# Kernel tuning notes

Hardware: AMD Instinct MI355X
Metric: run time of the kernel (lower is better)

## Reference

```python
import jax, jax.numpy as jnp
import numpy as np

ALPHA = 0.1
DEPTH = 10

N_NODES = 100000
N_EDGES = 3200000
FEATS = 512
HIDDEN = 64
CLASSES = 32


def setup_inputs() -> dict:
    key = jax.random.key(0)
    k1, k2, k3, k4 = jax.random.split(key, 4)
    x = jax.random.normal(k1, (N_NODES, FEATS), dtype=jnp.float32)
    edges = jax.random.randint(k2, (2, N_EDGES), 0, N_NODES, dtype=jnp.int64)
    # Linear weights (stored as [in, out] so forward is x @ W + b)
    W1 = jax.random.normal(k3, (FEATS, HIDDEN), dtype=jnp.float32) * (1.0 / np.sqrt(FEATS))
    b1 = jnp.zeros((HIDDEN,), dtype=jnp.float32)
    W2 = jax.random.normal(k4, (HIDDEN, CLASSES), dtype=jnp.float32) * (1.0 / np.sqrt(HIDDEN))
    b2 = jnp.zeros((CLASSES,), dtype=jnp.float32)
    return {"x": x, "edges": edges, "W1": W1, "b1": b1, "W2": W2, "b2": b2}


def reference(x, edges, W1, b1, W2, b2):
    # Eval mode: all dropouts (feature + edge) are identity.
    n = x.shape[0]
    src, dst = edges[0], edges[1]

    # Symmetric normalization 1/sqrt(deg_src * deg_dst), degrees from in-edges.
    deg = jax.ops.segment_sum(jnp.ones_like(dst, dtype=x.dtype), dst, num_segments=n)
    deg = jnp.maximum(deg, 1.0)
    norm = jax.lax.rsqrt(deg[src] * deg[dst])  # [E]

    # MLP: feats -> hidden -> classes
    h = jax.nn.relu(x @ W1 + b1) @ W2 + b2  # [N, classes]
    h0 = h

    # APPNP propagation: x <- (1-alpha) * A_hat x + alpha * h0
    for _ in range(DEPTH):
        msg = h[src] * norm[:, None]                          # gather  [E, classes]
        agg = jax.ops.segment_sum(msg, dst, num_segments=n)   # scatter [N, classes]
        h = agg * (1.0 - ALPHA) + ALPHA * h0
    return h
```

## Files before the change

kernel.cpp:

```cpp
#include <hip/hip_runtime.h>

#define ALPHA_F 0.1f
#define DEPTH 10
#define FEATS 512
#define CLS 32

__device__ __forceinline__ unsigned bf16rne(float f) {
  unsigned u = __float_as_uint(f);
  return (u + 0x7fffu + ((u >> 16) & 1u)) >> 16;
}
__device__ __forceinline__ float blo(unsigned q) { return __uint_as_float(q << 16); }
__device__ __forceinline__ float bhi(unsigned q) { return __uint_as_float(q & 0xffff0000u); }

__global__ __launch_bounds__(256) void k_deg(const int* __restrict__ dst, int E, int N,
                                             unsigned* __restrict__ deg,
                                             unsigned* __restrict__ rank) {
  int i = blockIdx.x * 256 + threadIdx.x;
  if (i >= E) return;
  int d = dst[i];
  unsigned r = 0;
  if ((unsigned)d < (unsigned)N) r = atomicAdd(&deg[d], 1u);
  rank[i] = r;
}

__global__ __launch_bounds__(1024) void k_scanp(const unsigned* __restrict__ deg, int N,
                                                unsigned* __restrict__ rowst2) {
  __shared__ unsigned sums[1024];
  int t = threadIdx.x;
  int chunk = (N + 1023) >> 10;
  int beg = t * chunk;
  int end = min(beg + chunk, N);
  unsigned s = 0;
  for (int i = beg; i < end; ++i) s += (deg[i] + 15u) & ~15u;
  sums[t] = s;
  __syncthreads();
  for (int off = 1; off < 1024; off <<= 1) {
    unsigned v = (t >= off) ? sums[t - off] : 0u;
    __syncthreads();
    sums[t] += v;
    __syncthreads();
  }
  unsigned pre = (t == 0) ? 0u : sums[t - 1];
  for (int i = beg; i < end; ++i) { rowst2[i] = pre; pre += (deg[i] + 15u) & ~15u; }
  if (t == 1023) rowst2[N] = pre;
}

__global__ __launch_bounds__(256) void k_colinit(unsigned* __restrict__ col2, int cap, int N) {
  int i = blockIdx.x * 256 + threadIdx.x;
  if (i < cap) col2[i] = (unsigned)N;
}

__global__ __launch_bounds__(256) void k_fill(const int* __restrict__ src,
                                              const int* __restrict__ dst,
                                              const unsigned* __restrict__ rank,
                                              const unsigned* __restrict__ rowst2,
                                              int E, int N,
                                              unsigned* __restrict__ col2) {
  int e = blockIdx.x * 256 + threadIdx.x;
  if (e >= E) return;
  int s = src[e];
  int d = dst[e];
  if ((unsigned)s >= (unsigned)N || (unsigned)d >= (unsigned)N) return;
  col2[rowst2[d] + rank[e]] = (unsigned)s;
}

__global__ __launch_bounds__(256) void k_mlp(const float* __restrict__ x,
                                             const float* __restrict__ W1,
                                             const float* __restrict__ b1,
                                             const float* __restrict__ W2,
                                             const float* __restrict__ b2,
                                             const unsigned* __restrict__ deg,
                                             unsigned short* __restrict__ h0b,
                                             unsigned short* __restrict__ u0,
                                             float* __restrict__ rs, int N) {
  __shared__ float XHs[64 * 65];
  __shared__ float W2s[64 * 32];
  __shared__ float b1s[64];
  __shared__ float b2s[32];
  int t = threadIdx.x;
  int m0 = blockIdx.x * 64;

  for (int i = t; i < 64 * 32; i += 256) W2s[i] = W2[i];
  if (t < 64) b1s[t] = b1[t];
  if (t < 32) b2s[t] = b2[t];

  int c = t & 31;
  int h = t >> 5;
  float acc[8][2];
#pragma unroll
  for (int i = 0; i < 8; ++i) { acc[i][0] = 0.f; acc[i][1] = 0.f; }

  for (int k0 = 0; k0 < FEATS; k0 += 64) {
    __syncthreads();
#pragma unroll
    for (int j = 0; j < 2; ++j) {
      int F = j * 256 + t;
      int r = F >> 3, q = F & 7;
      int row = m0 + r;
      float4 v = make_float4(0.f, 0.f, 0.f, 0.f);
      if (row < N) v = *(const float4*)(x + (size_t)row * FEATS + k0 + q * 8);
      *(float4*)(XHs + r * 64 + q * 8) = v;
      float4 v2 = make_float4(0.f, 0.f, 0.f, 0.f);
      if (row < N) v2 = *(const float4*)(x + (size_t)row * FEATS + k0 + q * 8 + 4);
      *(float4*)(XHs + r * 64 + q * 8 + 4) = v2;
    }
    __syncthreads();
    const float* W1p = W1 + (size_t)k0 * 64;
#pragma unroll
    for (int k4 = 0; k4 < 16; ++k4) {
      int k = k4 * 4;
      float4 xv[8];
#pragma unroll
      for (int i = 0; i < 8; ++i) xv[i] = *(const float4*)(XHs + (h * 8 + i) * 64 + k);
#pragma unroll
      for (int j = 0; j < 4; ++j) {
        float w0 = W1p[(k + j) * 64 + c];
        float w1 = W1p[(k + j) * 64 + c + 32];
#pragma unroll
        for (int i = 0; i < 8; ++i) {
          float xx = ((const float*)&xv[i])[j];
          acc[i][0] += xx * w0;
          acc[i][1] += xx * w1;
        }
      }
    }
  }
  __syncthreads();
#pragma unroll
  for (int i = 0; i < 8; ++i) {
    int r = h * 8 + i;
    float v0 = acc[i][0] + b1s[c];
    float v1 = acc[i][1] + b1s[c + 32];
    XHs[r * 65 + c] = v0 > 0.f ? v0 : 0.f;
    XHs[r * 65 + c + 32] = v1 > 0.f ? v1 : 0.f;
  }
  __syncthreads();
  int cc = t & 31;
#pragma unroll
  for (int i = 0; i < 8; ++i) {
    int r = h * 8 + i;
    float s = b2s[cc];
#pragma unroll
    for (int k = 0; k < 64; ++k) s += XHs[r * 65 + k] * W2s[k * 32 + cc];
    int row = m0 + r;
    if (row < N) {
      float dv = (float)deg[row];
      float rsv = rsqrtf(fmaxf(dv, 1.0f));
      h0b[(size_t)row * CLS + cc] = (unsigned short)bf16rne(s);
      u0[(size_t)row * CLS + cc] = (unsigned short)bf16rne(rsv * s);
      if (cc == 0) rs[row] = rsv;
    }
  }
}

template <bool LAST>
__global__ __launch_bounds__(256) void k_prop(const unsigned* __restrict__ u_in,
                                              const unsigned short* __restrict__ h0b,
                                              const float* __restrict__ rs,
                                              const unsigned* __restrict__ rowst2,
                                              const unsigned* __restrict__ col2,
                                              void* __restrict__ out, int N) {
  int t = blockIdx.x * 256 + threadIdx.x;
  int g = t >> 2;
  if (g >= N) return;
  int l = t & 3;
  unsigned beg = rowst2[g];
  unsigned end = rowst2[g + 1];
  const uint4* up = (const uint4*)u_in + l;
  const uint4* colv = (const uint4*)col2;
  float a[8];
#pragma unroll
  for (int j = 0; j < 8; ++j) a[j] = 0.f;
  for (unsigned e = beg; e < end; e += 16) {
    unsigned e4 = e >> 2;
    uint4 c0 = colv[e4 + 0];
    uint4 c1 = colv[e4 + 1];
    uint4 c2 = colv[e4 + 2];
    uint4 c3 = colv[e4 + 3];
    uint4 q0 = up[(size_t)c0.x * 4];
    uint4 q1 = up[(size_t)c0.y * 4];
    uint4 q2 = up[(size_t)c0.z * 4];
    uint4 q3 = up[(size_t)c0.w * 4];
    uint4 q4 = up[(size_t)c1.x * 4];
    uint4 q5 = up[(size_t)c1.y * 4];
    uint4 q6 = up[(size_t)c1.z * 4];
    uint4 q7 = up[(size_t)c1.w * 4];
    uint4 q8 = up[(size_t)c2.x * 4];
    uint4 q9 = up[(size_t)c2.y * 4];
    uint4 qa = up[(size_t)c2.z * 4];
    uint4 qb = up[(size_t)c2.w * 4];
    uint4 qc = up[(size_t)c3.x * 4];
    uint4 qd = up[(size_t)c3.y * 4];
    uint4 qe = up[(size_t)c3.z * 4];
    uint4 qf = up[(size_t)c3.w * 4];
#define ACC(q) \
    a[0] += blo(q.x); a[1] += bhi(q.x); a[2] += blo(q.y); a[3] += bhi(q.y); \
    a[4] += blo(q.z); a[5] += bhi(q.z); a[6] += blo(q.w); a[7] += bhi(q.w);
    ACC(q0) ACC(q1) ACC(q2) ACC(q3) ACC(q4) ACC(q5) ACC(q6) ACC(q7)
    ACC(q8) ACC(q9) ACC(qa) ACC(qb) ACC(qc) ACC(qd) ACC(qe) ACC(qf)
#undef ACC
  }
  float rsv = rs[g];
  uint4 hq = *((const uint4*)h0b + (size_t)g * 4 + l);
  float h0v[8] = { blo(hq.x), bhi(hq.x), blo(hq.y), bhi(hq.y),
                   blo(hq.z), bhi(hq.z), blo(hq.w), bhi(hq.w) };
  if (LAST) {
    float ca = ALPHA_F, cb = (1.0f - ALPHA_F) * rsv;
    float* op = (float*)out + (size_t)g * CLS + l * 8;
    *(float4*)(op) = make_float4(ca * h0v[0] + cb * a[0], ca * h0v[1] + cb * a[1],
                                 ca * h0v[2] + cb * a[2], ca * h0v[3] + cb * a[3]);
    *(float4*)(op + 4) = make_float4(ca * h0v[4] + cb * a[4], ca * h0v[5] + cb * a[5],
                                     ca * h0v[6] + cb * a[6], ca * h0v[7] + cb * a[7]);
  } else {
    float ca = ALPHA_F * rsv, cb = (1.0f - ALPHA_F) * rsv * rsv;
    float o[8];
#pragma unroll
    for (int j = 0; j < 8; ++j) o[j] = ca * h0v[j] + cb * a[j];
    uint4 p;
    p.x = bf16rne(o[0]) | (bf16rne(o[1]) << 16);
    p.y = bf16rne(o[2]) | (bf16rne(o[3]) << 16);
    p.z = bf16rne(o[4]) | (bf16rne(o[5]) << 16);
    p.w = bf16rne(o[6]) | (bf16rne(o[7]) << 16);
    *((uint4*)out + (size_t)g * 4 + l) = p;
  }
}

extern "C" void kernel_launch(void* const* d_in, const int* in_sizes, int n_in,
                              void* d_out, int out_size, void* d_ws, size_t ws_size,
                              hipStream_t stream) {
  const float* x = (const float*)d_in[0];
  const int* edges = (const int*)d_in[1];
  const float* W1 = (const float*)d_in[2];
  const float* b1 = (const float*)d_in[3];
  const float* W2 = (const float*)d_in[4];
  const float* b2 = (const float*)d_in[5];
  int N = in_sizes[0] / FEATS;
  int E = in_sizes[1] / 2;
  const int* src = edges;
  const int* dst = edges + E;
  int cap = E + 16 * N;

  char* ws = (char*)d_ws;
  auto align64 = [](size_t v) { return (v + 63) & ~(size_t)63; };
  size_t o = 0;
  unsigned* deg = (unsigned*)(ws + o);    o = align64(o + (size_t)N * 4);
  unsigned* rowst2 = (unsigned*)(ws + o); o = align64(o + (size_t)(N + 1) * 4);
  float* rs = (float*)(ws + o);           o = align64(o + (size_t)N * 4);
  unsigned* rank = (unsigned*)(ws + o);   o = align64(o + (size_t)E * 4);
  unsigned* col2 = (unsigned*)(ws + o);   o = align64(o + (size_t)cap * 4);
  unsigned short* h0b = (unsigned short*)(ws + o); o = align64(o + (size_t)N * CLS * 2);
  unsigned* uA = (unsigned*)(ws + o);     o = align64(o + (size_t)(N + 1) * CLS * 2);
  unsigned* uB = (unsigned*)(ws + o);     o = align64(o + (size_t)(N + 1) * CLS * 2);

  hipMemsetAsync(deg, 0, (size_t)N * 4, stream);
  hipMemsetAsync(uA + (size_t)N * 16, 0, 64, stream);
  hipMemsetAsync(uB + (size_t)N * 16, 0, 64, stream);
  k_deg<<<(E + 255) / 256, 256, 0, stream>>>(dst, E, N, deg, rank);
  k_scanp<<<1, 1024, 0, stream>>>(deg, N, rowst2);
  k_colinit<<<(cap + 255) / 256, 256, 0, stream>>>(col2, cap, N);
  k_fill<<<(E + 255) / 256, 256, 0, stream>>>(src, dst, rank, rowst2, E, N, col2);
  k_mlp<<<(N + 63) / 64, 256, 0, stream>>>(x, W1, b1, W2, b2, deg, h0b,
                                           (unsigned short*)uA, rs, N);

  float* outF = (float*)d_out;
  const unsigned* uin = uA;
  for (int it = 0; it < DEPTH - 1; ++it) {
    unsigned* uo = (it & 1) ? uA : uB;
    k_prop<false><<<((N * 4) + 255) / 256, 256, 0, stream>>>(uin, h0b, rs, rowst2, col2,
                                                             uo, N);
    uin = uo;
  }
  k_prop<true><<<((N * 4) + 255) / 256, 256, 0, stream>>>(uin, h0b, rs, rowst2, col2,
                                                          outF, N);
}
```

Before: 1.120 ms.

## Use split-bf16 MFMA for first MLP layer and fp16 propagation storage

The first linear layer moves from scalar FP32 FMAs to bf16 MFMA instructions. Both x and W1 are split into high and low bf16 parts, and three products are summed to keep accuracy close to FP32. K tiles shrink to 32 and shared memory is reorganised into padded hi/lo tiles. The stored propagation features and h0 switch from bf16 to fp16 to improve precision at the same bandwidth. This adds conversion work and more shared-memory traffic in the MLP, while the propagation kernels stay about the same cost.

```diff
diff --git a/kernel.cpp b/kernel.cpp
--- a/kernel.cpp
+++ b/kernel.cpp
@@ -1,16 +1,32 @@
 #include <hip/hip_runtime.h>
+#include <hip/hip_fp16.h>
 
 #define ALPHA_F 0.1f
 #define DEPTH 10
 #define FEATS 512
 #define CLS 32
 
+typedef __attribute__((ext_vector_type(8))) short short8v;
+typedef __attribute__((ext_vector_type(4))) short short4v;
+typedef __attribute__((ext_vector_type(4))) float f32x4;
+
 __device__ __forceinline__ unsigned bf16rne(float f) {
   unsigned u = __float_as_uint(f);
   return (u + 0x7fffu + ((u >> 16) & 1u)) >> 16;
 }
-__device__ __forceinline__ float blo(unsigned q) { return __uint_as_float(q << 16); }
-__device__ __forceinline__ float bhi(unsigned q) { return __uint_as_float(q & 0xffff0000u); }
+__device__ __forceinline__ float f16l(unsigned q) {
+  __half_raw r; r.x = (unsigned short)(q & 0xffffu);
+  return __half2float(*reinterpret_cast<const __half*>(&r));
+}
+__device__ __forceinline__ float f16h(unsigned q) { return f16l(q >> 16); }
+__device__ __forceinline__ unsigned f16pk(float a, float b) {
+  __half2 h = __floats2half2_rn(a, b);
+  return *reinterpret_cast<unsigned*>(&h);
+}
+__device__ __forceinline__ unsigned short f16u(float a) {
+  __half h = __float2half_rn(a);
+  return *reinterpret_cast<unsigned short*>(&h);
+}
 
 __global__ __launch_bounds__(256) void k_deg(const int* __restrict__ dst, int E, int N,
                                              unsigned* __restrict__ deg,
@@ -70,84 +86,116 @@
                                              const float* __restrict__ W2,
                                              const float* __restrict__ b2,
                                              const unsigned* __restrict__ deg,
-                                             unsigned short* __restrict__ h0b,
+                                             unsigned short* __restrict__ h0h,
                                              unsigned short* __restrict__ u0,
                                              float* __restrict__ rs, int N) {
-  __shared__ float XHs[64 * 65];
+  __shared__ __align__(16) unsigned char SB[18432];
   __shared__ float W2s[64 * 32];
   __shared__ float b1s[64];
   __shared__ float b2s[32];
+  unsigned short* Ahi = (unsigned short*)SB;
+  unsigned short* Alo = (unsigned short*)(SB + 4608);
+  unsigned short* Bhi = (unsigned short*)(SB + 9216);
+  unsigned short* Blo = (unsigned short*)(SB + 13824);
+  float* Hs = (float*)SB;
+
   int t = threadIdx.x;
   int m0 = blockIdx.x * 64;
-
   for (int i = t; i < 64 * 32; i += 256) W2s[i] = W2[i];
   if (t < 64) b1s[t] = b1[t];
   if (t < 32) b2s[t] = b2[t];
 
-  int c = t & 31;
-  int h = t >> 5;
-  float acc[8][2];
-#pragma unroll
-  for (int i = 0; i < 8; ++i) { acc[i][0] = 0.f; acc[i][1] = 0.f; }
-
-  for (int k0 = 0; k0 < FEATS; k0 += 64) {
+  int lane = t & 63, w = t >> 6;
+  int lr = lane & 15, kb = lane >> 4;
+  f32x4 acc[4];
+#pragma unroll
+  for (int n = 0; n < 4; ++n) acc[n] = (f32x4){0.f, 0.f, 0.f, 0.f};
+
+  int sr = t >> 2, sq = t & 3;
+  int wk = t >> 3, wc = (t & 7) * 8;
+
+  for (int k0 = 0; k0 < FEATS; k0 += 32) {
     __syncthreads();
-#pragma unroll
-    for (int j = 0; j < 2; ++j) {
-      int F = j * 256 + t;
-      int r = F >> 3, q = F & 7;
-      int row = m0 + r;
-      float4 v = make_float4(0.f, 0.f, 0.f, 0.f);
-      if (row < N) v = *(const float4*)(x + (size_t)row * FEATS + k0 + q * 8);
-      *(float4*)(XHs + r * 64 + q * 8) = v;
-      float4 v2 = make_float4(0.f, 0.f, 0.f, 0.f);
-      if (row < N) v2 = *(const float4*)(x + (size_t)row * FEATS + k0 + q * 8 + 4);
-      *(float4*)(XHs + r * 64 + q * 8 + 4) = v2;
+    {
+      int row = m0 + sr;
+      const float* gp = x + (size_t)row * FEATS + k0 + sq * 8;
+      float4 v0 = make_float4(0.f, 0.f, 0.f, 0.f), v1 = v0;
+      if (row < N) { v0 = *(const float4*)gp; v1 = *(const float4*)(gp + 4); }
+      float f[8] = {v0.x, v0.y, v0.z, v0.w, v1.x, v1.y, v1.z, v1.w};
+      unsigned short hh[8], ll[8];
+#pragma unroll
+      for (int j = 0; j < 8; ++j) {
+        unsigned hb = bf16rne(f[j]);
+        float fh = __uint_as_float(hb << 16);
+        hh[j] = (unsigned short)hb;
+        ll[j] = (unsigned short)bf16rne(f[j] - fh);
+      }
+      int base = sr * 36 + sq * 8;
+      *(ushort4*)(Ahi + base)     = make_ushort4(hh[0], hh[1], hh[2], hh[3]);
+      *(ushort4*)(Ahi + base + 4) = make_ushort4(hh[4], hh[5], hh[6], hh[7]);
+      *(ushort4*)(Alo + base)     = make_ushort4(ll[0], ll[1], ll[2], ll[3]);
+      *(ushort4*)(Alo + base + 4) = make_ushort4(ll[4], ll[5], ll[6], ll[7]);
+    }
+    {
+      const float* wp = W1 + (size_t)(k0 + wk) * 64 + wc;
+      float4 a0 = *(const float4*)wp, a1 = *(const float4*)(wp + 4);
+      float g[8] = {a0.x, a0.y, a0.z, a0.w, a1.x, a1.y, a1.z, a1.w};
+#pragma unroll
+      for (int j = 0; j < 8; ++j) {
+        unsigned hb = bf16rne(g[j]);
+        float fh = __uint_as_float(hb << 16);
+        Bhi[(wc + j) * 36 + wk] = (unsigned short)hb;
+        Blo[(wc + j) * 36 + wk] = (unsigned short)bf16rne(g[j] - fh);
+      }
     }
     __syncthreads();
-    const float* W1p = W1 + (size_t)k0 * 64;
-#pragma unroll
-    for (int k4 = 0; k4 < 16; ++k4) {
-      int k = k4 * 4;
-      float4 xv[8];
-#pragma unroll
-      for (int i = 0; i < 8; ++i) xv[i] = *(const float4*)(XHs + (h * 8 + i) * 64 + k);
-#pragma unroll
-      for (int j = 0; j < 4; ++j) {
-        float w0 = W1p[(k + j) * 64 + c];
-        float w1 = W1p[(k + j) * 64 + c + 32];
-#pragma unroll
-        for (int i = 0; i < 8; ++i) {
-          float xx = ((const float*)&xv[i])[j];
-          acc[i][0] += xx * w0;
-          acc[i][1] += xx * w1;
-        }
-      }
+    int abase = (w * 16 + lr) * 36 + kb * 8;
+    short4v a0h = *(short4v*)(Ahi + abase);
+    short4v a1h = *(short4v*)(Ahi + abase + 4);
+    short4v a0l = *(short4v*)(Alo + abase);
+    short4v a1l = *(short4v*)(Alo + abase + 4);
+    short8v ahi = __builtin_shufflevector(a0h, a1h, 0, 1, 2, 3, 4, 5, 6, 7);
+    short8v alo = __builtin_shufflevector(a0l, a1l, 0, 1, 2, 3, 4, 5, 6, 7);
+#pragma unroll
+    for (int n = 0; n < 4; ++n) {
+      int bbase = (n * 16 + lr) * 36 + kb * 8;
+      short4v b0h = *(short4v*)(Bhi + bbase);
+      short4v b1h = *(short4v*)(Bhi + bbase + 4);
+      short4v b0l = *(short4v*)(Blo + bbase);
+      short4v b1l = *(short4v*)(Blo + bbase + 4);
+      short8v bhi = __builtin_shufflevector(b0h, b1h, 0, 1, 2, 3, 4, 5, 6, 7);
+      short8v blo = __builtin_shufflevector(b0l, b1l, 0, 1, 2, 3, 4, 5, 6, 7);
+      acc[n] = __builtin_amdgcn_mfma_f32_16x16x32_bf16(ahi, bhi, acc[n], 0, 0, 0);
+      acc[n] = __builtin_amdgcn_mfma_f32_16x16x32_bf16(ahi, blo, acc[n], 0, 0, 0);
+      acc[n] = __builtin_amdgcn_mfma_f32_16x16x32_bf16(alo, bhi, acc[n], 0, 0, 0);
     }
   }
   __syncthreads();
 #pragma unroll
+  for (int n = 0; n < 4; ++n) {
+    int col = n * 16 + lr;
+    float bv = b1s[col];
+#pragma unroll
+    for (int j = 0; j < 4; ++j) {
+      int row = w * 16 + kb * 4 + j;
+      float v = acc[n][j] + bv;
+      Hs[row * 65 + col] = v > 0.f ? v : 0.f;
+    }
+  }
+  __syncthreads();
+  int cc = t & 31, hgrp = t >> 5;
+#pragma unroll
   for (int i = 0; i < 8; ++i) {
-    int r = h * 8 + i;
-    float v0 = acc[i][0] + b1s[c];
-    float v1 = acc[i][1] + b1s[c + 32];
-    XHs[r * 65 + c] = v0 > 0.f ? v0 : 0.f;
-    XHs[r * 65 + c + 32] = v1 > 0.f ? v1 : 0.f;
-  }
-  __syncthreads();
-  int cc = t & 31;
-#pragma unroll
-  for (int i = 0; i < 8; ++i) {
-    int r = h * 8 + i;
+    int r = hgrp * 8 + i;
     float s = b2s[cc];
 #pragma unroll
-    for (int k = 0; k < 64; ++k) s += XHs[r * 65 + k] * W2s[k * 32 + cc];
+    for (int k = 0; k < 64; ++k) s += Hs[r * 65 + k] * W2s[k * 32 + cc];
     int row = m0 + r;
     if (row < N) {
       float dv = (float)deg[row];
       float rsv = rsqrtf(fmaxf(dv, 1.0f));
-      h0b[(size_t)row * CLS + cc] = (unsigned short)bf16rne(s);
-      u0[(size_t)row * CLS + cc] = (unsigned short)bf16rne(rsv * s);
+      h0h[(size_t)row * CLS + cc] = f16u(s);
+      u0[(size_t)row * CLS + cc] = f16u(rsv * s);
       if (cc == 0) rs[row] = rsv;
     }
   }
@@ -155,7 +203,7 @@
 
 template <bool LAST>
 __global__ __launch_bounds__(256) void k_prop(const unsigned* __restrict__ u_in,
-                                              const unsigned short* __restrict__ h0b,
+                                              const unsigned short* __restrict__ h0h,
                                               const float* __restrict__ rs,
                                               const unsigned* __restrict__ rowst2,
                                               const unsigned* __restrict__ col2,
@@ -194,16 +242,16 @@
     uint4 qe = up[(size_t)c3.z * 4];
     uint4 qf = up[(size_t)c3.w * 4];
 #define ACC(q) \
-    a[0] += blo(q.x); a[1] += bhi(q.x); a[2] += blo(q.y); a[3] += bhi(q.y); \
-    a[4] += blo(q.z); a[5] += bhi(q.z); a[6] += blo(q.w); a[7] += bhi(q.w);
+    a[0] += f16l(q.x); a[1] += f16h(q.x); a[2] += f16l(q.y); a[3] += f16h(q.y); \
+    a[4] += f16l(q.z); a[5] += f16h(q.z); a[6] += f16l(q.w); a[7] += f16h(q.w);
     ACC(q0) ACC(q1) ACC(q2) ACC(q3) ACC(q4) ACC(q5) ACC(q6) ACC(q7)
     ACC(q8) ACC(q9) ACC(qa) ACC(qb) ACC(qc) ACC(qd) ACC(qe) ACC(qf)
 #undef ACC
   }
   float rsv = rs[g];
-  uint4 hq = *((const uint4*)h0b + (size_t)g * 4 + l);
-  float h0v[8] = { blo(hq.x), bhi(hq.x), blo(hq.y), bhi(hq.y),
-                   blo(hq.z), bhi(hq.z), blo(hq.w), bhi(hq.w) };
+  uint4 hq = *((const uint4*)h0h + (size_t)g * 4 + l);
+  float h0v[8] = { f16l(hq.x), f16h(hq.x), f16l(hq.y), f16h(hq.y),
+                   f16l(hq.z), f16h(hq.z), f16l(hq.w), f16h(hq.w) };
   if (LAST) {
     float ca = ALPHA_F, cb = (1.0f - ALPHA_F) * rsv;
     float* op = (float*)out + (size_t)g * CLS + l * 8;
@@ -217,10 +265,10 @@
 #pragma unroll
     for (int j = 0; j < 8; ++j) o[j] = ca * h0v[j] + cb * a[j];
     uint4 p;
-    p.x = bf16rne(o[0]) | (bf16rne(o[1]) << 16);
-    p.y = bf16rne(o[2]) | (bf16rne(o[3]) << 16);
-    p.z = bf16rne(o[4]) | (bf16rne(o[5]) << 16);
-    p.w = bf16rne(o[6]) | (bf16rne(o[7]) << 16);
+    p.x = f16pk(o[0], o[1]);
+    p.y = f16pk(o[2], o[3]);
+    p.z = f16pk(o[4], o[5]);
+    p.w = f16pk(o[6], o[7]);
     *((uint4*)out + (size_t)g * 4 + l) = p;
   }
 }
@@ -248,7 +296,7 @@
   float* rs = (float*)(ws + o);           o = align64(o + (size_t)N * 4);
   unsigned* rank = (unsigned*)(ws + o);   o = align64(o + (size_t)E * 4);
   unsigned* col2 = (unsigned*)(ws + o);   o = align64(o + (size_t)cap * 4);
-  unsigned short* h0b = (unsigned short*)(ws + o); o = align64(o + (size_t)N * CLS * 2);
+  unsigned short* h0h = (unsigned short*)(ws + o); o = align64(o + (size_t)N * CLS * 2);
   unsigned* uA = (unsigned*)(ws + o);     o = align64(o + (size_t)(N + 1) * CLS * 2);
   unsigned* uB = (unsigned*)(ws + o);     o = align64(o + (size_t)(N + 1) * CLS * 2);
 
@@ -259,17 +307,17 @@
   k_scanp<<<1, 1024, 0, stream>>>(deg, N, rowst2);
   k_colinit<<<(cap + 255) / 256, 256, 0, stream>>>(col2, cap, N);
   k_fill<<<(E + 255) / 256, 256, 0, stream>>>(src, dst, rank, rowst2, E, N, col2);
-  k_mlp<<<(N + 63) / 64, 256, 0, stream>>>(x, W1, b1, W2, b2, deg, h0b,
+  k_mlp<<<(N + 63) / 64, 256, 0, stream>>>(x, W1, b1, W2, b2, deg, h0h,
                                            (unsigned short*)uA, rs, N);
 
   float* outF = (float*)d_out;
   const unsigned* uin = uA;
   for (int it = 0; it < DEPTH - 1; ++it) {
     unsigned* uo = (it & 1) ? uA : uB;
-    k_prop<false><<<((N * 4) + 255) / 256, 256, 0, stream>>>(uin, h0b, rs, rowst2, col2,
+    k_prop<false><<<((N * 4) + 255) / 256, 256, 0, stream>>>(uin, h0h, rs, rowst2, col2,
                                                              uo, N);
     uin = uo;
   }
-  k_prop<true><<<((N * 4) + 255) / 256, 256, 0, stream>>>(uin, h0b, rs, rowst2, col2,
+  k_prop<true><<<((N * 4) + 255) / 256, 256, 0, stream>>>(uin, h0h, rs, rowst2, col2,
                                                           outF, N);
 }
```

Measured after the change: 1.068 ms. -4.6%, faster.
